# Kernel optimization log

Hardware: AMD Instinct MI355X
Metric: run time of the kernel (lower is better)

The kernel has to match this reference:

```python
import jax, jax.numpy as jnp
import numpy as np

B, N, C, K = 2, 8192, 128, 16

def _mlp2(h, W1, b1, W2, b2):
    return jax.nn.relu(h @ W1 + b1) @ W2 + b2

def setup_inputs() -> dict:
    key = jax.random.key(0)
    ks = jax.random.split(key, 20)
    s = lambda d: 1.0 / np.sqrt(d)
    inp = {
        "x": jax.random.normal(ks[0], (B, N, C), jnp.float32),
        "position": jax.random.normal(ks[1], (B, N, 3), jnp.float32),
        "Wq": jax.random.normal(ks[2], (C, C), jnp.float32) * s(C),
        "bq": jnp.zeros((C,), jnp.float32),
        "Wk": jax.random.normal(ks[3], (C, C), jnp.float32) * s(C),
        "bk": jnp.zeros((C,), jnp.float32),
        "Wv": jax.random.normal(ks[4], (C, C), jnp.float32) * s(C),
        "bv": jnp.zeros((C,), jnp.float32),
        "Wp1": jax.random.normal(ks[5], (3, C), jnp.float32) * s(3),
        "bp1": jnp.zeros((C,), jnp.float32),
        "Wp2": jax.random.normal(ks[6], (C, C), jnp.float32) * s(C),
        "bp2": jnp.zeros((C,), jnp.float32),
        "Wg1": jax.random.normal(ks[7], (C, C), jnp.float32) * s(C),
        "bg1": jnp.zeros((C,), jnp.float32),
        "Wg2": jax.random.normal(ks[8], (C, C), jnp.float32) * s(C),
        "bg2": jnp.zeros((C,), jnp.float32),
    }
    return inp

def reference(x, position, Wq, bq, Wk, bk, Wv, bv, Wp1, bp1, Wp2, bp2, Wg1, bg1, Wg2, bg2):
    # kNN via squared pairwise distances (monotone in cdist, same topk indices)
    p2 = jnp.sum(position * position, axis=-1)                       # (B,N)
    d2 = p2[:, :, None] + p2[:, None, :] - 2.0 * jnp.einsum("bnd,bmd->bnm", position, position)
    _, idx = jax.lax.top_k(-d2, K)                                    # (B,N,K) nearest (incl self)

    gather = jax.vmap(lambda arr, i: arr[i])                          # per-batch fancy gather
    neighbors = gather(x, idx)                                        # (B,N,K,C)
    pos_nb = gather(position, idx)                                    # (B,N,K,3)

    q = x @ Wq + bq                                                   # (B,N,C)
    k = neighbors @ Wk + bk                                           # (B,N,K,C)
    v = neighbors @ Wv + bv                                           # (B,N,K,C)

    # positional MLP only at gathered pairs (same math as all-pairs-then-gather)
    rel = position[:, :, None, :] - pos_nb                            # (B,N,K,3)
    pe = _mlp2(rel, Wp1, bp1, Wp2, bp2)                               # (B,N,K,C)

    scale = 1.0 / jnp.sqrt(jnp.float32(C))
    attn = (q[:, :, None, :] - k + pe) * scale
    attn = _mlp2(attn, Wg1, bg1, Wg2, bg2)
    attn = jax.nn.softmax(attn, axis=2)                               # softmax over K neighbors
    out = jnp.sum(attn * (v + pe), axis=2)                            # (B,N,C)
    return out
```

## Files before the change

### kernel.cpp

```cpp
#include <hip/hip_runtime.h>
#include <stdint.h>

#define NPTS 8192
#define CDIM 128
#define KNNK 16
#define WPAD 136
#define WELEMF 16384
#define SCALE 0.08838834764831845f
#define FLDS_BYTES 76800
#define GRES 32
#define NCELL (GRES*GRES*GRES)

typedef __attribute__((ext_vector_type(4))) float f32x4;
typedef __attribute__((ext_vector_type(8))) short s16x8;

__device__ __forceinline__ unsigned short to_bf16(float f){
  union { float f; unsigned int u; } v; v.f = f;
  return (unsigned short)((v.u + 0x7fffu + ((v.u >> 16) & 1u)) >> 16);
}

__device__ __forceinline__ s16x8 cvt8(const float* p){
  float4 lo = *(const float4*)p;
  float4 hi = *(const float4*)(p + 4);
  s16x8 f;
  f[0]=(short)to_bf16(lo.x); f[1]=(short)to_bf16(lo.y);
  f[2]=(short)to_bf16(lo.z); f[3]=(short)to_bf16(lo.w);
  f[4]=(short)to_bf16(hi.x); f[5]=(short)to_bf16(hi.y);
  f[6]=(short)to_bf16(hi.z); f[7]=(short)to_bf16(hi.w);
  return f;
}

__device__ __forceinline__ unsigned mapf_u(unsigned s){
  return s ^ (0x80000000u | (unsigned)(((int)s) >> 31));
}
__device__ __forceinline__ float unmapf_u(unsigned u){
  unsigned r = (u & 0x80000000u) ? (u ^ 0x80000000u) : ~u;
  return __uint_as_float(r);
}

__global__ __launch_bounds__(256) void zero_init_kernel(int* __restrict__ counts,
                                                        unsigned* __restrict__ bbox)
{
  int t = blockIdx.x*256 + threadIdx.x;
  if (t < 2*NCELL) counts[t] = 0;
  if (t < 12) bbox[t] = ((t % 6) < 3) ? 0xFFFFFFFFu : 0u;
}

__global__ __launch_bounds__(256) void prep_kernel(
    const float* __restrict__ Wq, const float* __restrict__ Wk,
    const float* __restrict__ Wv, const float* __restrict__ Wp2,
    const float* __restrict__ Wg1, const float* __restrict__ Wg2,
    const float* __restrict__ pos,
    unsigned short* __restrict__ wt, float4* __restrict__ pos4,
    unsigned* __restrict__ bbox)
{
  int t = blockIdx.x*256 + threadIdx.x;
  if (t < 6*WELEMF){
    int w = t >> 14, f = t & (WELEMF-1);
    int i = f & 7, ln = (f >> 3) & 63, kkct = f >> 9;
    int kk = kkct & 3, ct = kkct >> 2;
    int kdim = kk*32 + (ln >> 4)*8 + i, col = ct*16 + (ln & 15);
    const float* src = (w==0)?Wq:(w==1)?Wk:(w==2)?Wv:(w==3)?Wp2:(w==4)?Wg1:Wg2;
    float v = src[kdim*CDIM + col];
    if (w == 1) v = -v;
    wt[t] = to_bf16(v);
  } else {
    int m = t - 6*WELEMF;
    float xx = pos[m*3+0], yy = pos[m*3+1], zz = pos[m*3+2];
    float p2 = __fadd_rn(__fadd_rn(__fmul_rn(xx,xx), __fmul_rn(yy,yy)), __fmul_rn(zz,zz));
    pos4[m] = make_float4(xx, yy, zz, p2);
    unsigned mnx = mapf_u(__float_as_uint(xx)), mny = mapf_u(__float_as_uint(yy)), mnz = mapf_u(__float_as_uint(zz));
    unsigned mxx = mnx, mxy = mny, mxz = mnz;
#pragma unroll
    for (int off = 1; off < 64; off <<= 1){
      mnx = min(mnx, (unsigned)__shfl_xor((int)mnx, off));
      mny = min(mny, (unsigned)__shfl_xor((int)mny, off));
      mnz = min(mnz, (unsigned)__shfl_xor((int)mnz, off));
      mxx = max(mxx, (unsigned)__shfl_xor((int)mxx, off));
      mxy = max(mxy, (unsigned)__shfl_xor((int)mxy, off));
      mxz = max(mxz, (unsigned)__shfl_xor((int)mxz, off));
    }
    if ((threadIdx.x & 63) == 0){
      int b = m >> 13;
      atomicMin(&bbox[b*6+0], mnx); atomicMin(&bbox[b*6+1], mny); atomicMin(&bbox[b*6+2], mnz);
      atomicMax(&bbox[b*6+3], mxx); atomicMax(&bbox[b*6+4], mxy); atomicMax(&bbox[b*6+5], mxz);
    }
  }
}

__global__ __launch_bounds__(256) void bin_count_kernel(
    const float4* __restrict__ pos4, const unsigned* __restrict__ bbox,
    int* __restrict__ counts, int* __restrict__ cellId)
{
  int m = blockIdx.x*256 + threadIdx.x;
  int b = m >> 13;
  float4 p = pos4[m];
  float lox = unmapf_u(bbox[b*6+0]), loy = unmapf_u(bbox[b*6+1]), loz = unmapf_u(bbox[b*6+2]);
  float hix = unmapf_u(bbox[b*6+3]), hiy = unmapf_u(bbox[b*6+4]), hiz = unmapf_u(bbox[b*6+5]);
  int ix = min(GRES-1, max(0, (int)((p.x - lox) * ((float)GRES/(hix-lox)))));
  int iy = min(GRES-1, max(0, (int)((p.y - loy) * ((float)GRES/(hiy-loy)))));
  int iz = min(GRES-1, max(0, (int)((p.z - loz) * ((float)GRES/(hiz-loz)))));
  int cid = (iz*GRES + iy)*GRES + ix;
  cellId[m] = cid;
  atomicAdd(&counts[b*NCELL + cid], 1);
}

__global__ __launch_bounds__(1024) void scan_kernel(
    const int* __restrict__ counts, int* __restrict__ starts, int* __restrict__ cursor)
{
  __shared__ int part[1024];
  int b = blockIdx.x, t = threadIdx.x;
  const int* c = counts + b*NCELL;
  int* s = starts + b*(NCELL+1);
  int* cur = cursor + b*NCELL;
  int base = t*32, sum = 0;
  for (int i = 0; i < 32; ++i) sum += c[base+i];
  part[t] = sum; __syncthreads();
  for (int off = 1; off < 1024; off <<= 1){
    int v = (t >= off) ? part[t-off] : 0;
    __syncthreads();
    part[t] += v;
    __syncthreads();
  }
  int run = (t > 0) ? part[t-1] : 0;
  for (int i = 0; i < 32; ++i){ int cc = c[base+i]; s[base+i] = run; cur[base+i] = run; run += cc; }
  if (t == 1023) s[NCELL] = run;
}

__global__ __launch_bounds__(256) void scatter_kernel(
    const float4* __restrict__ pos4, const int* __restrict__ cellId,
    int* __restrict__ cursor, float4* __restrict__ spos4)
{
  int m = blockIdx.x*256 + threadIdx.x;
  int b = m >> 13;
  float4 p = pos4[m];
  int dst = atomicAdd(&cursor[b*NCELL + cellId[m]], 1);
  spos4[(b<<13) + dst] = make_float4(p.x, p.y, p.z, __uint_as_float((unsigned)(m & (NPTS-1))));
}

__global__ __launch_bounds__(256) void knn_grid_kernel(
    const float4* __restrict__ pos4, const float4* __restrict__ spos4,
    const int* __restrict__ starts, const unsigned* __restrict__ bbox,
    int* __restrict__ idxout)
{
  const int tid = threadIdx.x, lane = tid & 63;
  const int g = blockIdx.x*4 + (tid >> 6);
  const int b = g >> 13, n = g & (NPTS-1);
  const float4 q = pos4[((size_t)b<<13) + n];
  const float4* sp = spos4 + ((size_t)b<<13);
  const int*    st = starts + b*(NCELL+1);

  float lox = unmapf_u(bbox[b*6+0]), loy = unmapf_u(bbox[b*6+1]), loz = unmapf_u(bbox[b*6+2]);
  float hix = unmapf_u(bbox[b*6+3]), hiy = unmapf_u(bbox[b*6+4]), hiz = unmapf_u(bbox[b*6+5]);
  float cwx = (hix-lox)*(1.0f/GRES), cwy = (hiy-loy)*(1.0f/GRES), cwz = (hiz-loz)*(1.0f/GRES);
  int cx = min(GRES-1, max(0, (int)((q.x - lox) * ((float)GRES/(hix-lox)))));
  int cy = min(GRES-1, max(0, (int)((q.y - loy) * ((float)GRES/(hiy-loy)))));
  int cz = min(GRES-1, max(0, (int)((q.z - loz) * ((float)GRES/(hiz-loz)))));

  unsigned khi = 0xFFFFFFFFu, klo = 0xFFFFFFFFu;
  float Tf = __builtin_inff();

  auto insert = [&](unsigned ihi, unsigned ilo){
    unsigned phi = (unsigned)__builtin_amdgcn_update_dpp(0, (int)khi, 0x111, 0xF, 0xF, false);
    unsigned plo = (unsigned)__builtin_amdgcn_update_dpp(0, (int)klo, 0x111, 0xF, 0xF, false);
    bool gt  = (khi > ihi) || (khi == ihi && klo > ilo);
    bool pgt = ((lane & 15) != 0) && ((phi > ihi) || (phi == ihi && plo > ilo));
    khi = gt ? (pgt ? phi : ihi) : khi;
    klo = gt ? (pgt ? plo : ilo) : klo;
  };
  auto updT = [&](){
    unsigned t15 = (unsigned)__builtin_amdgcn_readlane((int)khi, 15);
    Tf = (t15 >= 0xFF800000u) ? __builtin_inff() : unmapf_u(t15);
  };

  for (int R = 1; R <= GRES-1; ++R){
    const bool first = (R == 1);
    const int per = 8*R, w1 = 2*R-1;
    const int ntask = first ? 9 : (per + 2*w1*w1);
    for (int tb = 0; tb < ntask; tb += 64){
      int t = tb + lane;
      int dy = 0, dz = 0, gx0 = 0, gx1 = -1;
      bool valid = t < ntask;
      if (first){
        if (valid){ dy = t % 3 - 1; dz = t / 3 - 1; }
        gx0 = max(cx-1, 0); gx1 = min(cx+1, GRES-1);
      } else if (valid){
        if (t < per){
          int s2 = 2*(2*R+1);
          if (t < s2){ dz = (t < 2*R+1) ? -R : R; dy = t % (2*R+1) - R; }
          else { int u = t - s2; dy = (u & 1) ? R : -R; dz = (u >> 1) - (R-1); }
          gx0 = max(cx-R, 0); gx1 = min(cx+R, GRES-1);
        } else {
          int i = t - per, ri = i >> 1;
          dy = ri % w1 - (R-1); dz = ri / w1 - (R-1);
          int gx = cx + ((i & 1) ? R : -R);
          gx0 = gx; gx1 = gx;
          valid = gx >= 0 && gx <= GRES-1;
        }
      }
      int gy = cy + dy, gz = cz + dz;
      valid = valid && gy >= 0 && gy < GRES && gz >= 0 && gz < GRES && gx0 <= gx1;
      int s0 = 0, s1 = 0;
      if (valid){ int cb = (gz*GRES + gy)*GRES; s0 = st[cb + gx0]; s1 = st[cb + gx1 + 1]; }
      unsigned long long cm = __ballot(valid && (s1 > s0));
      while (cm){
        int sl = (int)__builtin_ctzll(cm); cm &= cm - 1;
        int cs = __builtin_amdgcn_readlane(s0, sl);
        int ce = __builtin_amdgcn_readlane(s1, sl);
        for (int p0 = cs; p0 < ce; p0 += 64){
          int mm = p0 + lane;
          bool v = mm < ce;
          float4 c = v ? sp[mm] : make_float4(0.f,0.f,0.f,0.f);
          float c2  = __fadd_rn(__fadd_rn(__fmul_rn(c.x,c.x), __fmul_rn(c.y,c.y)), __fmul_rn(c.z,c.z));
          float dot = __builtin_fmaf(c.z, q.z, __builtin_fmaf(c.y, q.y, __fmul_rn(c.x, q.x)));
          float d2  = __fsub_rn(__fadd_rn(q.w, c2), __fadd_rn(dot, dot));
          int oi = __float_as_int(c.w);
          bool ins = v && (d2 <= Tf);
          unsigned long long im = __ballot(ins);
          if (im){
            while (im){
              int s = (int)__builtin_ctzll(im); im &= im - 1;
              unsigned dvb = (unsigned)__builtin_amdgcn_readlane((int)__float_as_uint(d2), s);
              int ov = __builtin_amdgcn_readlane(oi, s);
              insert(mapf_u(dvb), (unsigned)ov);
            }
            updT();
          }
        }
      }
    }
    const float big = 1e30f;
    float dxlo = (cx-R <= 0)      ? big : (q.x - (lox + (float)(cx-R)*cwx));
    float dxhi = (cx+R >= GRES-1) ? big : ((lox + (float)(cx+R+1)*cwx) - q.x);
    float dylo = (cy-R <= 0)      ? big : (q.y - (loy + (float)(cy-R)*cwy));
    float dyhi = (cy+R >= GRES-1) ? big : ((loy + (float)(cy+R+1)*cwy) - q.y);
    float dzlo = (cz-R <= 0)      ? big : (q.z - (loz + (float)(cz-R)*cwz));
    float dzhi = (cz+R >= GRES-1) ? big : ((loz + (float)(cz+R+1)*cwz) - q.z);
    float dmin = fminf(fminf(fminf(dxlo,dxhi), fminf(dylo,dyhi)), fminf(dzlo,dzhi));
    if (dmin >= 1e29f) break;
    dmin = fmaxf(dmin, 0.0f);
    float dmin2 = dmin*dmin;
    if (Tf + 1e-4f + Tf*1e-5f < dmin2) break;
  }
  if (lane < KNNK) idxout[(size_t)g*KNNK + lane] = (int)klo;
}

__global__ __launch_bounds__(256, 2) void fused_kernel(
    const float* __restrict__ x, const float* __restrict__ pos,
    const float* __restrict__ bq, const float* __restrict__ bk,
    const float* __restrict__ bv, const float* __restrict__ Wp1,
    const float* __restrict__ bp1, const float* __restrict__ bp2,
    const float* __restrict__ bg1, const float* __restrict__ bg2,
    const int* __restrict__ idxws, const unsigned short* __restrict__ wt,
    float* __restrict__ out)
{
  extern __shared__ char smem[];
  char* Sbase = smem;
  char* Tbase = smem + 32768;
  unsigned short* t_base = (unsigned short*)Tbase;
  float* blds = (float*)(smem + 67584);
  float* q_lds = (float*)(smem + 72704);

  const int tid = threadIdx.x;
  const int lane = tid & 63, w = tid >> 6;
  const int r = lane & 15, grp = lane >> 4;
  const int pbase = blockIdx.x * 8;
  const int b = pbase >> 13;

  auto gll = [&](int s, char* dst){
#pragma unroll
    for (int k = 0; k < 8; ++k){
      int c = w*8 + k;
      unsigned short* g = const_cast<unsigned short*>(wt) + (size_t)s*WELEMF + c*512 + lane*8;
      __builtin_amdgcn_global_load_lds(
        (const __attribute__((address_space(1))) void*)g,
        (__attribute__((address_space(3))) void*)(dst + c*1024), 16, 0, 0);
    }
  };
  auto ldS = [&](int ct, int kk) -> s16x8 {
    return *(const s16x8*)&((unsigned short*)Sbase)[((ct*4 + kk)*64 + lane)*8];
  };
  auto ldT = [&](int ct, int kk) -> s16x8 {
    return *(const s16x8*)&((unsigned short*)Tbase)[((ct*4 + kk)*64 + lane)*8];
  };

  gll(0, Sbase);
  gll(3, Tbase);

  for (int e = tid; e < 1280; e += 256){
    float v;
    if      (e < 128)  v = bq[e];
    else if (e < 256)  v = bk[e-128];
    else if (e < 384)  v = bv[e-256];
    else if (e < 512)  v = bp2[e-384];
    else if (e < 640)  v = bg1[e-512];
    else if (e < 768)  v = bg2[e-640];
    else if (e < 896)  v = bp1[e-768];
    else               v = Wp1[e-896];
    blds[e] = v;
  }
  int nbr[2]; float relx[2], rely[2], relz[2];
#pragma unroll
  for (int j = 0; j < 2; ++j){
    int gp = pbase + w*2 + j;
    nbr[j] = idxws[(size_t)gp*KNNK + r];
    const float* pq = pos + (size_t)gp*3;
    const float* pn = pos + ((size_t)b*NPTS + nbr[j])*3;
    relx[j] = pq[0]-pn[0]; rely[j] = pq[1]-pn[1]; relz[j] = pq[2]-pn[2];
  }
  s16x8 qa[4];
  {
    const float* xr = x + (size_t)(pbase + (r & 7))*CDIM;
#pragma unroll
    for (int kk = 0; kk < 4; ++kk) qa[kk] = cvt8(xr + kk*32 + grp*8);
  }
  __syncthreads();

  {
    f32x4 qacc[2] = { {0.f,0.f,0.f,0.f}, {0.f,0.f,0.f,0.f} };
#pragma unroll
    for (int c2 = 0; c2 < 2; ++c2){
      int ct = w*2 + c2;
#pragma unroll
      for (int kk = 0; kk < 4; ++kk)
        qacc[c2] = __builtin_amdgcn_mfma_f32_16x16x32_bf16(qa[kk], ldS(ct,kk), qacc[c2], 0,0,0);
    }
#pragma unroll
    for (int c2 = 0; c2 < 2; ++c2){
      int col = (w*2+c2)*16 + r;
#pragma unroll
      for (int jj = 0; jj < 4; ++jj){
        int row = grp*4 + jj;
        if (row < 8) q_lds[row*CDIM + col] = qacc[c2][jj] + blds[col];
      }
    }
  }
  s16x8 pf[2][4];
#pragma unroll
  for (int j = 0; j < 2; ++j)
#pragma unroll
    for (int kk = 0; kk < 4; ++kk){
      s16x8 f;
#pragma unroll
      for (int i = 0; i < 8; ++i){
        int kc = kk*32 + grp*8 + i;
        float s = relx[j]*blds[896+kc] + rely[j]*blds[1024+kc] + relz[j]*blds[1152+kc] + blds[768+kc];
        f[i] = (short)to_bf16(fmaxf(s, 0.f));
      }
      pf[j][kk] = f;
    }
  __syncthreads();
  gll(1, Sbase);

  f32x4 at[2][8], av[2][8];
#pragma unroll
  for (int j=0;j<2;++j)
#pragma unroll
    for (int ct=0;ct<8;++ct) at[j][ct] = (f32x4){0.f,0.f,0.f,0.f};
#pragma unroll
  for (int ct=0;ct<8;++ct)
#pragma unroll
    for (int kk=0;kk<4;++kk){
      s16x8 bw = ldT(ct,kk);
#pragma unroll
      for (int j=0;j<2;++j)
        at[j][ct] = __builtin_amdgcn_mfma_f32_16x16x32_bf16(pf[j][kk], bw, at[j][ct], 0,0,0);
    }
  s16x8 nf[2][4];
#pragma unroll
  for (int j=0;j<2;++j)
#pragma unroll
    for (int kk=0;kk<4;++kk)
      nf[j][kk] = cvt8(x + ((size_t)b*NPTS + nbr[j])*CDIM + kk*32 + grp*8);

  __syncthreads();
  gll(2, Tbase);
#pragma unroll
  for (int j=0;j<2;++j)
#pragma unroll
    for (int ct=0;ct<8;++ct) av[j][ct] = at[j][ct];
#pragma unroll
  for (int ct=0;ct<8;++ct)
#pragma unroll
    for (int kk=0;kk<4;++kk){
      s16x8 bw = ldS(ct,kk);
#pragma unroll
      for (int j=0;j<2;++j) at[j][ct] = __builtin_amdgcn_mfma_f32_16x16x32_bf16(nf[j][kk], bw, at[j][ct], 0,0,0);
    }
  __syncthreads();
  gll(4, Sbase);
#pragma unroll
  for (int ct=0;ct<8;++ct)
#pragma unroll
    for (int kk=0;kk<4;++kk){
      s16x8 bw = ldT(ct,kk);
#pragma unroll
      for (int j=0;j<2;++j) av[j][ct] = __builtin_amdgcn_mfma_f32_16x16x32_bf16(nf[j][kk], bw, av[j][ct], 0,0,0);
    }
#pragma unroll
  for (int j=0;j<2;++j){
    int prow = (w*2+j)*CDIM;
#pragma unroll
    for (int ct=0;ct<8;++ct){
      int col = ct*16+r;
      float add = q_lds[prow+col] + blds[384+col] - blds[128+col];
#pragma unroll
      for (int jj=0;jj<4;++jj) at[j][ct][jj] = (at[j][ct][jj] + add)*SCALE;
    }
  }
  __syncthreads();

  unsigned short* tl = t_base + w*(2*16*WPAD);
#pragma unroll
  for (int j=0;j<2;++j)
#pragma unroll
    for (int ct=0;ct<8;++ct)
#pragma unroll
      for (int jj=0;jj<4;++jj)
        tl[(j*16 + grp*4+jj)*WPAD + ct*16 + r] = to_bf16(at[j][ct][jj]);
  s16x8 tf[2][4];
#pragma unroll
  for (int j=0;j<2;++j)
#pragma unroll
    for (int kk=0;kk<4;++kk)
      tf[j][kk] = *(const s16x8*)&tl[(j*16 + r)*WPAD + kk*32 + grp*8];
  f32x4 hacc[2][8];
#pragma unroll
  for (int j=0;j<2;++j)
#pragma unroll
    for (int ct=0;ct<8;++ct) hacc[j][ct] = (f32x4){0.f,0.f,0.f,0.f};
#pragma unroll
  for (int ct=0;ct<8;++ct)
#pragma unroll
    for (int kk=0;kk<4;++kk){
      s16x8 bw = ldS(ct,kk);
#pragma unroll
      for (int j=0;j<2;++j)
        hacc[j][ct] = __builtin_amdgcn_mfma_f32_16x16x32_bf16(tf[j][kk], bw, hacc[j][ct], 0,0,0);
    }
  __syncthreads();
  gll(5, Sbase);
#pragma unroll
  for (int j=0;j<2;++j)
#pragma unroll
    for (int ct=0;ct<8;++ct){
      int col = ct*16+r; float bb = blds[512+col];
#pragma unroll
      for (int jj=0;jj<4;++jj)
        tl[(j*16+grp*4+jj)*WPAD + ct*16 + r] = to_bf16(fmaxf(hacc[j][ct][jj]+bb, 0.f));
    }
  s16x8 hf[2][4];
#pragma unroll
  for (int j=0;j<2;++j)
#pragma unroll
    for (int kk=0;kk<4;++kk)
      hf[j][kk] = *(const s16x8*)&tl[(j*16 + r)*WPAD + kk*32 + grp*8];
  __syncthreads();
  f32x4 gacc[2][8];
#pragma unroll
  for (int j=0;j<2;++j)
#pragma unroll
    for (int ct=0;ct<8;++ct) gacc[j][ct] = (f32x4){0.f,0.f,0.f,0.f};
#pragma unroll
  for (int ct=0;ct<8;++ct)
#pragma unroll
    for (int kk=0;kk<4;++kk){
      s16x8 bw = ldS(ct,kk);
#pragma unroll
      for (int j=0;j<2;++j)
        gacc[j][ct] = __builtin_amdgcn_mfma_f32_16x16x32_bf16(hf[j][kk], bw, gacc[j][ct], 0,0,0);
    }
#pragma unroll
  for (int j=0;j<2;++j){
#pragma unroll
    for (int ct=0;ct<8;++ct){
      int col = ct*16+r;
      float gb = blds[640+col];
      float g0v = gacc[j][ct][0]+gb, g1v = gacc[j][ct][1]+gb;
      float g2v = gacc[j][ct][2]+gb, g3v = gacc[j][ct][3]+gb;
      float mx = fmaxf(fmaxf(g0v,g1v), fmaxf(g2v,g3v));
      mx = fmaxf(mx, __shfl_xor(mx,16));
      mx = fmaxf(mx, __shfl_xor(mx,32));
      float e0=__expf(g0v-mx), e1=__expf(g1v-mx), e2=__expf(g2v-mx), e3=__expf(g3v-mx);
      float vb = blds[256+col] + blds[384+col];
      float ss = e0+e1+e2+e3;
      float oo = e0*(av[j][ct][0]+vb) + e1*(av[j][ct][1]+vb)
               + e2*(av[j][ct][2]+vb) + e3*(av[j][ct][3]+vb);
      ss += __shfl_xor(ss,16); ss += __shfl_xor(ss,32);
      oo += __shfl_xor(oo,16); oo += __shfl_xor(oo,32);
      if (grp == 0) out[(size_t)(pbase + w*2 + j)*CDIM + col] = oo/ss;
    }
  }
}

extern "C" void kernel_launch(void* const* d_in, const int* in_sizes, int n_in,
                              void* d_out, int out_size, void* d_ws, size_t ws_size,
                              hipStream_t stream)
{
  const float* x    = (const float*)d_in[0];
  const float* pos  = (const float*)d_in[1];
  const float* Wq   = (const float*)d_in[2];
  const float* bq   = (const float*)d_in[3];
  const float* Wk   = (const float*)d_in[4];
  const float* bk   = (const float*)d_in[5];
  const float* Wv   = (const float*)d_in[6];
  const float* bv   = (const float*)d_in[7];
  const float* Wp1  = (const float*)d_in[8];
  const float* bp1  = (const float*)d_in[9];
  const float* Wp2  = (const float*)d_in[10];
  const float* bp2  = (const float*)d_in[11];
  const float* Wg1  = (const float*)d_in[12];
  const float* bg1  = (const float*)d_in[13];
  const float* Wg2  = (const float*)d_in[14];
  const float* bg2  = (const float*)d_in[15];
  float* out = (float*)d_out;

  char* ws = (char*)d_ws;
  int*            idxs   = (int*)ws;
  unsigned short* wt     = (unsigned short*)(ws + 1048576);
  float4*         pos4   = (float4*)(ws + 1257472);
  float4*         spos4  = (float4*)(ws + 1519616);
  int*            cellId = (int*)(ws + 1847296);
  int*            counts = (int*)(ws + 1912832);
  int*            starts = (int*)(ws + 2174976);
  int*            cursor = (int*)(ws + 2437376);
  unsigned*       bbox   = (unsigned*)(ws + 2699520);

  hipFuncSetAttribute((const void*)fused_kernel,
                      hipFuncAttributeMaxDynamicSharedMemorySize, FLDS_BYTES);

  zero_init_kernel<<<256, 256, 0, stream>>>(counts, bbox);
  prep_kernel<<<448, 256, 0, stream>>>(Wq, Wk, Wv, Wp2, Wg1, Wg2, pos, wt, pos4, bbox);
  bin_count_kernel<<<64, 256, 0, stream>>>(pos4, bbox, counts, cellId);
  scan_kernel<<<2, 1024, 0, stream>>>(counts, starts, cursor);
  scatter_kernel<<<64, 256, 0, stream>>>(pos4, cellId, cursor, spos4);
  knn_grid_kernel<<<4096, 256, 0, stream>>>(pos4, spos4, starts, bbox, idxs);
  fused_kernel<<<2048, 256, FLDS_BYTES, stream>>>(x, pos, bq, bk, bv, Wp1, bp1, bp2,
                                                  bg1, bg2, idxs, wt, out);
}
```

Baseline: 222.7 us.

## Coarsen kNN grid to 16^3 and iterate queries in cell-sorted order

Halves the spatial grid resolution, so each cell holds about eight times more points and the scan, zero-init and bookkeeping shrink to match. The kNN kernel now takes its queries from the cell-sorted position array and writes results back via the original index. Neighbouring waves therefore visit the same cells, which should improve cache locality and reduce divergence between waves. Coarser cells mean more candidate distance checks per query but fewer cell visits and ring iterations.

```diff
diff --git a/kernel.cpp b/kernel.cpp
--- a/kernel.cpp
+++ b/kernel.cpp
@@ -8,7 +8,7 @@
 #define WELEMF 16384
 #define SCALE 0.08838834764831845f
 #define FLDS_BYTES 76800
-#define GRES 32
+#define GRES 16
 #define NCELL (GRES*GRES*GRES)
 
 typedef __attribute__((ext_vector_type(4))) float f32x4;
@@ -113,8 +113,8 @@
   const int* c = counts + b*NCELL;
   int* s = starts + b*(NCELL+1);
   int* cur = cursor + b*NCELL;
-  int base = t*32, sum = 0;
-  for (int i = 0; i < 32; ++i) sum += c[base+i];
+  int base = t*4, sum = 0;
+  for (int i = 0; i < 4; ++i) sum += c[base+i];
   part[t] = sum; __syncthreads();
   for (int off = 1; off < 1024; off <<= 1){
     int v = (t >= off) ? part[t-off] : 0;
@@ -123,7 +123,7 @@
     __syncthreads();
   }
   int run = (t > 0) ? part[t-1] : 0;
-  for (int i = 0; i < 32; ++i){ int cc = c[base+i]; s[base+i] = run; cur[base+i] = run; run += cc; }
+  for (int i = 0; i < 4; ++i){ int cc = c[base+i]; s[base+i] = run; cur[base+i] = run; run += cc; }
   if (t == 1023) s[NCELL] = run;
 }
 
@@ -139,23 +139,26 @@
 }
 
 __global__ __launch_bounds__(256) void knn_grid_kernel(
-    const float4* __restrict__ pos4, const float4* __restrict__ spos4,
-    const int* __restrict__ starts, const unsigned* __restrict__ bbox,
-    int* __restrict__ idxout)
+    const float4* __restrict__ spos4, const int* __restrict__ starts,
+    const unsigned* __restrict__ bbox, int* __restrict__ idxout)
 {
   const int tid = threadIdx.x, lane = tid & 63;
   const int g = blockIdx.x*4 + (tid >> 6);
   const int b = g >> 13, n = g & (NPTS-1);
-  const float4 q = pos4[((size_t)b<<13) + n];
   const float4* sp = spos4 + ((size_t)b<<13);
   const int*    st = starts + b*(NCELL+1);
+
+  const float4 q4 = sp[n];
+  const int orig = __float_as_int(q4.w);
+  const float qx = q4.x, qy = q4.y, qz = q4.z;
+  const float q2 = __fadd_rn(__fadd_rn(__fmul_rn(qx,qx), __fmul_rn(qy,qy)), __fmul_rn(qz,qz));
 
   float lox = unmapf_u(bbox[b*6+0]), loy = unmapf_u(bbox[b*6+1]), loz = unmapf_u(bbox[b*6+2]);
   float hix = unmapf_u(bbox[b*6+3]), hiy = unmapf_u(bbox[b*6+4]), hiz = unmapf_u(bbox[b*6+5]);
   float cwx = (hix-lox)*(1.0f/GRES), cwy = (hiy-loy)*(1.0f/GRES), cwz = (hiz-loz)*(1.0f/GRES);
-  int cx = min(GRES-1, max(0, (int)((q.x - lox) * ((float)GRES/(hix-lox)))));
-  int cy = min(GRES-1, max(0, (int)((q.y - loy) * ((float)GRES/(hiy-loy)))));
-  int cz = min(GRES-1, max(0, (int)((q.z - loz) * ((float)GRES/(hiz-loz)))));
+  int cx = min(GRES-1, max(0, (int)((qx - lox) * ((float)GRES/(hix-lox)))));
+  int cy = min(GRES-1, max(0, (int)((qy - loy) * ((float)GRES/(hiy-loy)))));
+  int cz = min(GRES-1, max(0, (int)((qz - loz) * ((float)GRES/(hiz-loz)))));
 
   unsigned khi = 0xFFFFFFFFu, klo = 0xFFFFFFFFu;
   float Tf = __builtin_inff();
@@ -212,8 +215,8 @@
           bool v = mm < ce;
           float4 c = v ? sp[mm] : make_float4(0.f,0.f,0.f,0.f);
           float c2  = __fadd_rn(__fadd_rn(__fmul_rn(c.x,c.x), __fmul_rn(c.y,c.y)), __fmul_rn(c.z,c.z));
-          float dot = __builtin_fmaf(c.z, q.z, __builtin_fmaf(c.y, q.y, __fmul_rn(c.x, q.x)));
-          float d2  = __fsub_rn(__fadd_rn(q.w, c2), __fadd_rn(dot, dot));
+          float dot = __builtin_fmaf(c.z, qz, __builtin_fmaf(c.y, qy, __fmul_rn(c.x, qx)));
+          float d2  = __fsub_rn(__fadd_rn(q2, c2), __fadd_rn(dot, dot));
           int oi = __float_as_int(c.w);
           bool ins = v && (d2 <= Tf);
           unsigned long long im = __ballot(ins);
@@ -230,19 +233,19 @@
       }
     }
     const float big = 1e30f;
-    float dxlo = (cx-R <= 0)      ? big : (q.x - (lox + (float)(cx-R)*cwx));
-    float dxhi = (cx+R >= GRES-1) ? big : ((lox + (float)(cx+R+1)*cwx) - q.x);
-    float dylo = (cy-R <= 0)      ? big : (q.y - (loy + (float)(cy-R)*cwy));
-    float dyhi = (cy+R >= GRES-1) ? big : ((loy + (float)(cy+R+1)*cwy) - q.y);
-    float dzlo = (cz-R <= 0)      ? big : (q.z - (loz + (float)(cz-R)*cwz));
-    float dzhi = (cz+R >= GRES-1) ? big : ((loz + (float)(cz+R+1)*cwz) - q.z);
+    float dxlo = (cx-R <= 0)      ? big : (qx - (lox + (float)(cx-R)*cwx));
+    float dxhi = (cx+R >= GRES-1) ? big : ((lox + (float)(cx+R+1)*cwx) - qx);
+    float dylo = (cy-R <= 0)      ? big : (qy - (loy + (float)(cy-R)*cwy));
+    float dyhi = (cy+R >= GRES-1) ? big : ((loy + (float)(cy+R+1)*cwy) - qy);
+    float dzlo = (cz-R <= 0)      ? big : (qz - (loz + (float)(cz-R)*cwz));
+    float dzhi = (cz+R >= GRES-1) ? big : ((loz + (float)(cz+R+1)*cwz) - qz);
     float dmin = fminf(fminf(fminf(dxlo,dxhi), fminf(dylo,dyhi)), fminf(dzlo,dzhi));
     if (dmin >= 1e29f) break;
     dmin = fmaxf(dmin, 0.0f);
     float dmin2 = dmin*dmin;
     if (Tf + 1e-4f + Tf*1e-5f < dmin2) break;
   }
-  if (lane < KNNK) idxout[(size_t)g*KNNK + lane] = (int)klo;
+  if (lane < KNNK) idxout[(((size_t)b<<13) + orig)*KNNK + lane] = (int)klo;
 }
 
 __global__ __launch_bounds__(256, 2) void fused_kernel(
@@ -529,12 +532,12 @@
   hipFuncSetAttribute((const void*)fused_kernel,
                       hipFuncAttributeMaxDynamicSharedMemorySize, FLDS_BYTES);
 
-  zero_init_kernel<<<256, 256, 0, stream>>>(counts, bbox);
+  zero_init_kernel<<<32, 256, 0, stream>>>(counts, bbox);
   prep_kernel<<<448, 256, 0, stream>>>(Wq, Wk, Wv, Wp2, Wg1, Wg2, pos, wt, pos4, bbox);
   bin_count_kernel<<<64, 256, 0, stream>>>(pos4, bbox, counts, cellId);
   scan_kernel<<<2, 1024, 0, stream>>>(counts, starts, cursor);
   scatter_kernel<<<64, 256, 0, stream>>>(pos4, cellId, cursor, spos4);
-  knn_grid_kernel<<<4096, 256, 0, stream>>>(pos4, spos4, starts, bbox, idxs);
+  knn_grid_kernel<<<4096, 256, 0, stream>>>(spos4, starts, bbox, idxs);
   fused_kernel<<<2048, 256, FLDS_BYTES, stream>>>(x, pos, bq, bk, bv, Wp1, bp1, bp2,
                                                   bg1, bg2, idxs, wt, out);
 }
```

Result: no change. 220.6 us (-1.0%).
